# Kernel tuning notes

Hardware: AMD Instinct MI355X
Metric: run time of the kernel (lower is better)

The kernel has to match this reference:

```python
import jax, jax.numpy as jnp
import numpy as np

# Static skeleton structure (mirrors init_kwargs adj_list)
J = 25            # joints (second dim of x)
E = 24            # edges, sorted keys 0..23
DEG = 2           # neighbors per edge: adj[i] = [i, i+1]
P = E * DEG       # total (edge, neighbor) conv pairs = 48
CIN, COUT, K = 16, 16, 3
L = 65536
LOUT = L - K + 1  # VALID conv, stride 1 (torch Conv1d defaults)

# pair p = (edge p//DEG, neighbor index below) in edge-sorted order
PAIR_NBR = np.array([j for i in range(E) for j in (i, i + 1)], dtype=np.int32)  # (P,)


def setup_inputs() -> dict:
    key = jax.random.key(0)
    k1, k2, k3 = jax.random.split(key, 3)
    x = jax.random.normal(k1, (CIN, J, L), dtype=jnp.float32)
    # per-(edge,neighbor) Conv1d weights/biases, stacked in edge-sorted pair order
    W = jax.random.normal(k2, (P, COUT, CIN, K), dtype=jnp.float32) * 0.05
    b = jax.random.normal(k3, (P, COUT), dtype=jnp.float32) * 0.05
    return {"x": x, "W": W, "b": b}


def reference(x, W, b):
    # gather neighbor slices for every (edge, neighbor) pair: (CIN, P, L) -> (P, CIN, L)
    nbr = jnp.asarray(PAIR_NBR)
    xg = jnp.transpose(x[:, nbr, :], (1, 0, 2))
    # one grouped conv replaces P tiny Conv1d launches: groups = P
    lhs = xg.reshape(1, P * CIN, L)
    rhs = W.reshape(P * COUT, CIN, K)
    out = jax.lax.conv_general_dilated(
        lhs, rhs, window_strides=(1,), padding='VALID',
        feature_group_count=P, dimension_numbers=('NCH', 'OIH', 'NCH'))
    out = out.reshape(P, COUT, LOUT) + b[:, :, None]   # (P, COUT, LOUT)
    # average over each edge's neighbors (uniform degree DEG)
    y = out.reshape(E, DEG, COUT, LOUT).mean(axis=1)   # (E, COUT, LOUT)
    # torch stacks per-edge (COUT, LOUT) results at dim=1 -> (COUT, E, LOUT)
    return jnp.transpose(y, (1, 0, 2))
```

## Files before the change

### kernel.cpp

```cpp
#include <hip/hip_runtime.h>
#include <hip/hip_bf16.h>


#define NJ    25
#define LSEQ  65536
#define NE    24
#define LOUTN (LSEQ - 2)
#define CW    260

typedef __attribute__((ext_vector_type(8))) short bf16x8;
typedef __attribute__((ext_vector_type(4))) float f32x4;

static __device__ __forceinline__ unsigned cvtpk(float lo, float hi) {
    union { __hip_bfloat162 h; unsigned u; } cv;
    cv.h = __float22bfloat162_rn(make_float2(lo, hi));
    return cv.u;
}

__global__ __launch_bounds__(256)
void skel_mfma_kernel(const float* __restrict__ x,
                      const float* __restrict__ W,
                      const float* __restrict__ b,
                      float* __restrict__ out)
{
    __shared__ unsigned lds[16 * CW];

    const int e   = blockIdx.y;
    const int tb  = blockIdx.x * 256;
    const int tid = threadIdx.x;
    const int l   = tid & 63, wv = tid >> 6;
    const int g   = l >> 4,  lc = l & 15;

    const float* wp = W + ((size_t)((2 * e) * 16 + lc) * 16 + 4 * g) * 3;
    f32x4 wj0[3], wj1[3];
    #pragma unroll
    for (int q = 0; q < 3; ++q) {
        wj0[q] = *reinterpret_cast<const f32x4*>(wp + 4 * q);
        wj1[q] = *reinterpret_cast<const f32x4*>(wp + 768 + 4 * q);
    }
    union { unsigned u[4]; bf16x8 v8; } Aw[3];
    #pragma unroll
    for (int d = 0; d < 4; ++d)
        #pragma unroll
        for (int k = 0; k < 3; ++k) {
            const int f = d * 3 + k;
            Aw[k].u[d] = cvtpk(wj0[f >> 2][f & 3], wj1[f >> 2][f & 3]);
        }

    const f32x4 b0 = *reinterpret_cast<const f32x4*>(b + (size_t)(2 * e) * 16 + 4 * g);
    const f32x4 b1 = *reinterpret_cast<const f32x4*>(b + (size_t)(2 * e + 1) * 16 + 4 * g);
    f32x4 bias;
    #pragma unroll
    for (int r = 0; r < 4; ++r) bias[r] = 0.5f * (b0[r] + b1[r]);

    {
        const int rp = tid >> 4;
        const int q0 = tid & 15;
        const float* xlo = x + (size_t)(rp * NJ + e) * LSEQ + tb;
        #pragma unroll
        for (int s = 0; s < 4; ++s) {
            const int c = 4 * q0 + 64 * s;
            float4 lo = *reinterpret_cast<const float4*>(xlo + c);
            float4 hi = *reinterpret_cast<const float4*>(xlo + LSEQ + c);
            uint4 pk;
            pk.x = cvtpk(lo.x, hi.x);
            pk.y = cvtpk(lo.y, hi.y);
            pk.z = cvtpk(lo.z, hi.z);
            pk.w = cvtpk(lo.w, hi.w);
            *reinterpret_cast<uint4*>(&lds[rp * CW + c]) = pk;
        }
    }
    if (tid < 32) {
        const int rp = tid >> 1, h = tid & 1;
        const int gc = min(tb + 256 + h, LSEQ - 1);
        const float* xl = x + (size_t)(rp * NJ + e) * LSEQ;
        lds[rp * CW + 256 + h] = cvtpk(xl[gc], xl[gc + LSEQ]);
    }
    __syncthreads();

    #pragma unroll
    for (int tc = 0; tc < 4; ++tc) {
        const int cb = wv * 64 + tc * 16 + lc;
        f32x4 C = {0.f, 0.f, 0.f, 0.f};
        #pragma unroll
        for (int k = 0; k < 3; ++k) {
            union { unsigned u[4]; bf16x8 v8; } Bx;
            #pragma unroll
            for (int d = 0; d < 4; ++d)
                Bx.u[d] = lds[(4 * g + d) * CW + cb + k];
            C = __builtin_amdgcn_mfma_f32_16x16x32_bf16(Aw[k].v8, Bx.v8, C, 0, 0, 0);
        }

        const int t = tb + cb;
        if (t < LOUTN) {
            #pragma unroll
            for (int r = 0; r < 4; ++r)
                out[(size_t)((4 * g + r) * NE + e) * LOUTN + t] = fmaf(0.5f, C[r], bias[r]);
        }
    }
}

extern "C" void kernel_launch(void* const* d_in, const int* in_sizes, int n_in,
                              void* d_out, int out_size, void* d_ws, size_t ws_size,
                              hipStream_t stream)
{
    const float* x = (const float*)d_in[0];
    const float* W = (const float*)d_in[1];
    const float* b = (const float*)d_in[2];
    float* out     = (float*)d_out;

    dim3 grid((LOUTN + 255) / 256, NE);
    skel_mfma_kernel<<<grid, 256, 0, stream>>>(x, W, b, out);
}
```

Baseline: 42.86 us.

## Process four chunks per block with register prefetch of the next chunk

Each block now walks four consecutive 256-column chunks instead of one, and the grid shrinks by four in x. While the current chunk is being computed, the global loads for the next chunk are issued into registers, which overlaps load latency with MFMA work and store issue. This also amortizes the per-block weight and bias loading and the bf16 conversion. The costs are extra registers for the prefetch buffers, an extra barrier per chunk, and fewer blocks to hide latency in a kernel that is already close to memory bandwidth.

```diff
diff --git a/kernel.cpp b/kernel.cpp
--- a/kernel.cpp
+++ b/kernel.cpp
@@ -7,6 +7,7 @@
 #define NE    24
 #define LOUTN (LSEQ - 2)
 #define CW    260
+#define CPB   4
 
 typedef __attribute__((ext_vector_type(8))) short bf16x8;
 typedef __attribute__((ext_vector_type(4))) float f32x4;
@@ -26,7 +27,7 @@
     __shared__ unsigned lds[16 * CW];
 
     const int e   = blockIdx.y;
-    const int tb  = blockIdx.x * 256;
+    const int cb0 = blockIdx.x * (CPB * 256);
     const int tid = threadIdx.x;
     const int l   = tid & 63, wv = tid >> 6;
     const int g   = l >> 4,  lc = l & 15;
@@ -53,50 +54,75 @@
     #pragma unroll
     for (int r = 0; r < 4; ++r) bias[r] = 0.5f * (b0[r] + b1[r]);
 
-    {
-        const int rp = tid >> 4;
-        const int q0 = tid & 15;
-        const float* xlo = x + (size_t)(rp * NJ + e) * LSEQ + tb;
+    const int rp = tid >> 4;
+    const int q0 = tid & 15;
+    const float* xrow = x + (size_t)(rp * NJ + e) * LSEQ;
+    const int hrp = tid >> 1, hh = tid & 1;
+    const float* xh = x + (size_t)(hrp * NJ + e) * LSEQ;
+
+    float4 PL[4], PH[4];
+    float hl0 = 0.f, hl1 = 0.f;
+
+    auto issue_loads = [&](int tb) {
+        const float* xlo = xrow + tb;
         #pragma unroll
         for (int s = 0; s < 4; ++s) {
             const int c = 4 * q0 + 64 * s;
-            float4 lo = *reinterpret_cast<const float4*>(xlo + c);
-            float4 hi = *reinterpret_cast<const float4*>(xlo + LSEQ + c);
+            PL[s] = *reinterpret_cast<const float4*>(xlo + c);
+            PH[s] = *reinterpret_cast<const float4*>(xlo + LSEQ + c);
+        }
+        if (tid < 32) {
+            const int gc = min(tb + 256 + hh, LSEQ - 1);
+            hl0 = xh[gc]; hl1 = xh[gc + LSEQ];
+        }
+    };
+
+    auto write_lds = [&]() {
+        #pragma unroll
+        for (int s = 0; s < 4; ++s) {
+            const int c = 4 * q0 + 64 * s;
             uint4 pk;
-            pk.x = cvtpk(lo.x, hi.x);
-            pk.y = cvtpk(lo.y, hi.y);
-            pk.z = cvtpk(lo.z, hi.z);
-            pk.w = cvtpk(lo.w, hi.w);
+            pk.x = cvtpk(PL[s].x, PH[s].x);
+            pk.y = cvtpk(PL[s].y, PH[s].y);
+            pk.z = cvtpk(PL[s].z, PH[s].z);
+            pk.w = cvtpk(PL[s].w, PH[s].w);
             *reinterpret_cast<uint4*>(&lds[rp * CW + c]) = pk;
         }
-    }
-    if (tid < 32) {
-        const int rp = tid >> 1, h = tid & 1;
-        const int gc = min(tb + 256 + h, LSEQ - 1);
-        const float* xl = x + (size_t)(rp * NJ + e) * LSEQ;
-        lds[rp * CW + 256 + h] = cvtpk(xl[gc], xl[gc + LSEQ]);
-    }
-    __syncthreads();
+        if (tid < 32) lds[hrp * CW + 256 + hh] = cvtpk(hl0, hl1);
+    };
+
+    issue_loads(cb0);
 
     #pragma unroll
-    for (int tc = 0; tc < 4; ++tc) {
-        const int cb = wv * 64 + tc * 16 + lc;
-        f32x4 C = {0.f, 0.f, 0.f, 0.f};
+    for (int cc = 0; cc < CPB; ++cc) {
+        const int tb = cb0 + cc * 256;
+
+        write_lds();
+        __syncthreads();
+
+        if (cc + 1 < CPB) issue_loads(tb + 256);
+
         #pragma unroll
-        for (int k = 0; k < 3; ++k) {
-            union { unsigned u[4]; bf16x8 v8; } Bx;
+        for (int tc = 0; tc < 4; ++tc) {
+            const int cb = wv * 64 + tc * 16 + lc;
+            f32x4 C = {0.f, 0.f, 0.f, 0.f};
             #pragma unroll
-            for (int d = 0; d < 4; ++d)
-                Bx.u[d] = lds[(4 * g + d) * CW + cb + k];
-            C = __builtin_amdgcn_mfma_f32_16x16x32_bf16(Aw[k].v8, Bx.v8, C, 0, 0, 0);
+            for (int k = 0; k < 3; ++k) {
+                union { unsigned u[4]; bf16x8 v8; } Bx;
+                #pragma unroll
+                for (int d = 0; d < 4; ++d)
+                    Bx.u[d] = lds[(4 * g + d) * CW + cb + k];
+                C = __builtin_amdgcn_mfma_f32_16x16x32_bf16(Aw[k].v8, Bx.v8, C, 0, 0, 0);
+            }
+            const int t = tb + cb;
+            if (t < LOUTN) {
+                #pragma unroll
+                for (int r = 0; r < 4; ++r)
+                    out[(size_t)((4 * g + r) * NE + e) * LOUTN + t] = fmaf(0.5f, C[r], bias[r]);
+            }
         }
 
-        const int t = tb + cb;
-        if (t < LOUTN) {
-            #pragma unroll
-            for (int r = 0; r < 4; ++r)
-                out[(size_t)((4 * g + r) * NE + e) * LOUTN + t] = fmaf(0.5f, C[r], bias[r]);
-        }
+        if (cc + 1 < CPB) __syncthreads();
     }
 }
 
@@ -109,6 +135,6 @@
     const float* b = (const float*)d_in[2];
     float* out     = (float*)d_out;
 
-    dim3 grid((LOUTN + 255) / 256, NE);
+    dim3 grid((LOUTN + CPB * 256 - 1) / (CPB * 256), NE);
     skel_mfma_kernel<<<grid, 256, 0, stream>>>(x, W, b, out);
 }
```

After: 42.86 us. No clear change (+0.0%).

## Stage MFMA outputs in LDS and emit aligned vectorized float4 global stores

Applied to the files above, without the earlier changes.

Instead of each lane writing scalar floats straight from MFMA accumulators, results are written to LDS with a per-row shift so that each output row's global start is 16-element aligned. They are then read back and written to global memory as float4 stores, with scalar fallback at the edges. This targets the store-bound output path (output rows have odd length LOUTN, so they are misaligned) at the cost of extra LDS traffic, two more barriers and more LDS use per block.

```diff
diff --git a/kernel.cpp b/kernel.cpp
--- a/kernel.cpp
+++ b/kernel.cpp
@@ -7,6 +7,8 @@
 #define NE    24
 #define LOUTN (LSEQ - 2)
 #define CW    260
+#define CWT   292
+#define LDSN  (64 + 16 * CWT)
 
 typedef __attribute__((ext_vector_type(8))) short bf16x8;
 typedef __attribute__((ext_vector_type(4))) float f32x4;
@@ -23,7 +25,7 @@
                       const float* __restrict__ b,
                       float* __restrict__ out)
 {
-    __shared__ unsigned lds[16 * CW];
+    __shared__ unsigned lds[LDSN];
 
     const int e   = blockIdx.y;
     const int tb  = blockIdx.x * 256;
@@ -78,24 +80,62 @@
     }
     __syncthreads();
 
+    f32x4 C[4];
     #pragma unroll
     for (int tc = 0; tc < 4; ++tc) {
         const int cb = wv * 64 + tc * 16 + lc;
-        f32x4 C = {0.f, 0.f, 0.f, 0.f};
+        f32x4 acc = {0.f, 0.f, 0.f, 0.f};
         #pragma unroll
         for (int k = 0; k < 3; ++k) {
             union { unsigned u[4]; bf16x8 v8; } Bx;
             #pragma unroll
             for (int d = 0; d < 4; ++d)
                 Bx.u[d] = lds[(4 * g + d) * CW + cb + k];
-            C = __builtin_amdgcn_mfma_f32_16x16x32_bf16(Aw[k].v8, Bx.v8, C, 0, 0, 0);
+            acc = __builtin_amdgcn_mfma_f32_16x16x32_bf16(Aw[k].v8, Bx.v8, acc, 0, 0, 0);
         }
+        C[tc] = acc;
+    }
+    __syncthreads();
 
-        const int t = tb + cb;
-        if (t < LOUTN) {
+    {
+        float* cl = reinterpret_cast<float*>(lds);
+        int srw[4];
+        #pragma unroll
+        for (int r = 0; r < 4; ++r) {
+            const int row = 4 * g + r;
+            const size_t rb = (size_t)(row * NE + e) * LOUTN + tb;
+            srw[r] = (int)((16 - (rb & 15)) & 15);
+        }
+        #pragma unroll
+        for (int tc = 0; tc < 4; ++tc) {
+            const int cb = wv * 64 + tc * 16 + lc;
             #pragma unroll
             for (int r = 0; r < 4; ++r)
-                out[(size_t)((4 * g + r) * NE + e) * LOUTN + t] = fmaf(0.5f, C[r], bias[r]);
+                cl[64 + (4 * g + r) * CWT + 16 + cb - srw[r]] = fmaf(0.5f, C[tc][r], bias[r]);
+        }
+    }
+    __syncthreads();
+
+    {
+        const float* cl = reinterpret_cast<const float*>(lds);
+        const int row = tid >> 4;
+        const int q   = tid & 15;
+        const size_t rbase = (size_t)(row * NE + e) * LOUTN;
+        const int srow = (int)((16 - ((rbase + tb) & 15)) & 15);
+        #pragma unroll
+        for (int s = 0; s < 5; ++s) {
+            const int col = srow - 64 + 64 * s + 4 * q;
+            const f32x4 v = *reinterpret_cast<const f32x4*>(
+                cl + 64 + row * CWT - 48 + 64 * s + 4 * q);
+            const long t = (long)tb + col;
+            if (col >= 0 && col + 3 < 256 && t + 3 < LOUTN) {
+                *reinterpret_cast<f32x4*>(out + rbase + t) = v;
+            } else {
+                #pragma unroll
+                for (int d = 0; d < 4; ++d)
+                    if (col + d >= 0 && col + d < 256 && t + d < LOUTN)
+                        out[rbase + t + d] = v[d];
+            }
         }
     }
 }
```

Result: faster. 41.02 us (-4.3%).
